# Performance work log

Hardware: AMD Instinct MI355X
Metric: run time of the kernel (lower is better)

## Reference

```python
import jax, jax.numpy as jnp
import numpy as np

B, N, C, H = 2, 4096, 256, 4
DH = C // H  # 64
EPS = 1e-6
TEMPERATURE = 1.0


def setup_inputs() -> dict:
    key = jax.random.key(0)
    ks = jax.random.split(key, 12)
    s = 0.02
    return {
        "x": jax.random.normal(ks[0], (B, N, C), dtype=jnp.float32),
        "pos_embed": jax.random.normal(ks[1], (B, N, C), dtype=jnp.float32),
        # per-head Q/K/V linear weights stacked over heads (torch Linear(dim, dim_head))
        "Wq": jax.random.normal(ks[2], (H, C, DH), dtype=jnp.float32) * s,
        "bq": jax.random.normal(ks[3], (H, DH), dtype=jnp.float32) * s,
        "Wk": jax.random.normal(ks[4], (H, C, DH), dtype=jnp.float32) * s,
        "bk": jax.random.normal(ks[5], (H, DH), dtype=jnp.float32) * s,
        "Wv": jax.random.normal(ks[6], (H, C, DH), dtype=jnp.float32) * s,
        "bv": jax.random.normal(ks[7], (H, DH), dtype=jnp.float32) * s,
        "Wo": jax.random.normal(ks[8], (C, C), dtype=jnp.float32) * s,
        "bo": jax.random.normal(ks[9], (C,), dtype=jnp.float32) * s,
        "ln_g": jnp.ones((C,), dtype=jnp.float32),
        "ln_b": jnp.zeros((C,), dtype=jnp.float32),
    }


def reference(x, pos_embed, Wq, bq, Wk, bk, Wv, bv, Wo, bo, ln_g, ln_b):
    dk = TEMPERATURE * jnp.sqrt(jnp.float32(DH))
    # pre-norm: x + pos_embed -> dropout(p=0, identity) -> LayerNorm(eps=1e-6)
    h = x + pos_embed
    mu = jnp.mean(h, axis=-1, keepdims=True)
    var = jnp.mean(jnp.square(h - mu), axis=-1, keepdims=True)
    h = (h - mu) * jax.lax.rsqrt(var + EPS) * ln_g + ln_b  # [B,N,C]
    # all heads at once (original loops over heads with separate small Linears)
    q = jnp.einsum("bnc,hcd->bhnd", h, Wq) + bq[None, :, None, :]
    k = jnp.einsum("bnc,hcd->bhnd", h, Wk) + bk[None, :, None, :]
    v = jnp.einsum("bnc,hcd->bhnd", h, Wv) + bv[None, :, None, :]
    scores = jnp.einsum("bhid,bhjd->bhij", q, k) / dk  # [B,H,N,N]
    # NOTE: original uses F.softmax(dot_prod, dim=1) on [B,N,N] -> normalize over
    # the QUERY axis i, not the key axis j. Replicated faithfully here (axis=2).
    attn = jax.nn.softmax(scores, axis=2)
    o = jnp.einsum("bhij,bhjd->bhid", attn, v)  # [B,H,N,DH]
    o = jnp.transpose(o, (0, 2, 1, 3)).reshape(B, N, C)  # concat heads on channel
    return o @ Wo + bo
```

## Files before the change

kernel.cpp:

```cpp
#include <hip/hip_runtime.h>
#include <math.h>

#define B_ 2
#define N_ 4096
#define C_ 256
#define H_ 4
#define DH_ 64
#define EPS_ 1e-6f
#define SCALE_Q_ 0.18033688011112042f

typedef short bf16x8 __attribute__((ext_vector_type(8)));
typedef short bf16x4v __attribute__((ext_vector_type(4)));
typedef float f32x4 __attribute__((ext_vector_type(4)));
typedef int i32x4 __attribute__((ext_vector_type(4)));

#define MFMA32(a, b, c) __builtin_amdgcn_mfma_f32_16x16x32_bf16(a, b, c, 0, 0, 0)
#define FAST_EXP2(x) __builtin_amdgcn_exp2f(x)

__device__ __forceinline__ unsigned short f2bf(float x) {
  unsigned int u = __float_as_uint(x);
  return (unsigned short)((u + 0x7FFFu + ((u >> 16) & 1u)) >> 16);
}
__device__ __forceinline__ float bf2f(unsigned short u) {
  return __uint_as_float(((unsigned int)u) << 16);
}
__device__ __forceinline__ int pack2bf(float lo, float hi) {
  return (int)__builtin_amdgcn_perm(__float_as_uint(hi) + 0x8000u,
                                    __float_as_uint(lo) + 0x8000u, 0x07060302u);
}

__global__ __launch_bounds__(256) void ln_kernel(
    const float* __restrict__ x, const float* __restrict__ pos,
    const float* __restrict__ g, const float* __restrict__ beta,
    unsigned short* __restrict__ h16) {
  const int w = threadIdx.x >> 6, lane = threadIdx.x & 63;
  const int row = blockIdx.x * 4 + w;
  const float4 xv = *(const float4*)&x[row * C_ + lane * 4];
  const float4 pv = *(const float4*)&pos[row * C_ + lane * 4];
  float4 v = {xv.x + pv.x, xv.y + pv.y, xv.z + pv.z, xv.w + pv.w};
  float s = v.x + v.y + v.z + v.w;
  s += __shfl_xor(s, 1);  s += __shfl_xor(s, 2);  s += __shfl_xor(s, 4);
  s += __shfl_xor(s, 8);  s += __shfl_xor(s, 16); s += __shfl_xor(s, 32);
  const float mu = s * (1.0f / C_);
  float4 d = {v.x - mu, v.y - mu, v.z - mu, v.w - mu};
  float q = d.x * d.x + d.y * d.y + d.z * d.z + d.w * d.w;
  q += __shfl_xor(q, 1);  q += __shfl_xor(q, 2);  q += __shfl_xor(q, 4);
  q += __shfl_xor(q, 8);  q += __shfl_xor(q, 16); q += __shfl_xor(q, 32);
  const float rs = rsqrtf(q * (1.0f / C_) + EPS_);
  const float4 g4 = *(const float4*)&g[lane * 4];
  const float4 b4 = *(const float4*)&beta[lane * 4];
  bf16x4v o;
  o[0] = (short)f2bf(d.x * rs * g4.x + b4.x);
  o[1] = (short)f2bf(d.y * rs * g4.y + b4.y);
  o[2] = (short)f2bf(d.z * rs * g4.z + b4.z);
  o[3] = (short)f2bf(d.w * rs * g4.w + b4.w);
  *(bf16x4v*)&h16[row * C_ + lane * 4] = o;
}

__global__ __launch_bounds__(256) void wconv_kernel(
    const float* __restrict__ Wq, const float* __restrict__ Wk,
    const float* __restrict__ Wv, const float* __restrict__ Wo,
    unsigned short* __restrict__ W3T, unsigned short* __restrict__ WoT) {
  const int base = blockIdx.x * 2048;
#pragma unroll
  for (int p = 0; p < 8; p++) {
    const int idx = base + p * 256 + threadIdx.x;
    if (idx < 196608) {
      const int m = idx >> 14;
      const int rem = idx & 16383;
      const int c = rem >> 6, d = rem & 63;
      const int h = m / 3, kind = m - h * 3;
      const float* W = kind == 0 ? Wq : kind == 1 ? Wk : Wv;
      float v = W[h * 16384 + rem];
      if (kind == 0) v *= SCALE_Q_;
      W3T[(h * 192 + kind * 64 + d) * 256 + c] = f2bf(v);
    } else {
      const int widx = idx - 196608;
      const int k = widx >> 8, n = widx & 255;
      WoT[n * 256 + k] = f2bf(Wo[widx]);
    }
  }
}

__global__ __launch_bounds__(256) void qkv_kernel(
    const unsigned short* __restrict__ h16, const unsigned short* __restrict__ W3T,
    const float* __restrict__ bq, const float* __restrict__ bk,
    const float* __restrict__ bv,
    unsigned short* __restrict__ q16, unsigned short* __restrict__ k16,
    unsigned short* __restrict__ vT16) {
  const int rt = blockIdx.x;
  const int hh = blockIdx.y;
  const int t = threadIdx.x;
  const int w = t >> 6, lane = t & 63, c = lane & 15, quad = lane >> 4;
  __shared__ unsigned short Hs[64 * 64];
  __shared__ unsigned short Bs[192 * 64];
  const int row0 = rt * 64;

  f32x4 acc[12];
#pragma unroll
  for (int nt = 0; nt < 12; nt++) acc[nt] = (f32x4){0.f, 0.f, 0.f, 0.f};

  for (int kt = 0; kt < C_; kt += 64) {
    __syncthreads();
#pragma unroll
    for (int p = 0; p < 2; p++) {
      const int e = t + p * 256;
      const int row = e >> 3, ch = e & 7;
      *(bf16x8*)&Hs[row * 64 + ((ch ^ (row & 7)) * 8)] =
          *(const bf16x8*)&h16[(size_t)(row0 + row) * C_ + kt + ch * 8];
    }
#pragma unroll
    for (int p = 0; p < 6; p++) {
      const int e = t + p * 256;
      const int row = e >> 3, ch = e & 7;
      *(bf16x8*)&Bs[row * 64 + ((ch ^ (row & 7)) * 8)] =
          *(const bf16x8*)&W3T[(size_t)(hh * 192 + row) * C_ + kt + ch * 8];
    }
    __syncthreads();
#pragma unroll
    for (int kh = 0; kh < 2; kh++) {
      const int i = w * 16 + c;
      bf16x8 a = *(const bf16x8*)&Hs[i * 64 + (((kh * 4 + quad) ^ (i & 7)) * 8)];
#pragma unroll
      for (int nt = 0; nt < 12; nt++) {
        const int n = nt * 16 + c;
        bf16x8 b = *(const bf16x8*)&Bs[n * 64 + (((kh * 4 + quad) ^ (n & 7)) * 8)];
        acc[nt] = MFMA32(a, b, acc[nt]);
      }
    }
  }
#pragma unroll
  for (int nt = 0; nt < 12; nt++) {
    const int kind = nt >> 2;
    const int col = (nt & 3) * 16 + c;
    const float bias = kind == 0 ? bq[hh * 64 + col] * SCALE_Q_
                     : kind == 1 ? bk[hh * 64 + col] : bv[hh * 64 + col];
#pragma unroll
    for (int r = 0; r < 4; r++) {
      const int gr = row0 + w * 16 + quad * 4 + r;
      const int b = gr >> 12, n = gr & (N_ - 1);
      const size_t bh = (size_t)(b * H_ + hh);
      const unsigned short val = f2bf(acc[nt][r] + bias);
      if (kind == 0)      q16[(bh * N_ + n) * DH_ + col] = val;
      else if (kind == 1) k16[(bh * N_ + n) * DH_ + col] = val;
      else                vT16[(bh * DH_ + col) * N_ + n] = val;
    }
  }
}

__global__ __launch_bounds__(256, 2) void colstats_kernel(
    const unsigned short* __restrict__ q16, const unsigned short* __restrict__ k16,
    unsigned short* __restrict__ vT16) {
  const int blk = blockIdx.x;
  const int bh = blk & 7;
  const int j0 = (blk >> 3) * 64;
  const int t = threadIdx.x;
  const int w = t >> 6, lane = t & 63, c = lane & 15, quad = lane >> 4;
  __shared__ unsigned short Qs[64 * 64];
  __shared__ float Lp[4][64];
  __shared__ float ilv[64];

  bf16x8 ka[4][2];
#pragma unroll
  for (int jb = 0; jb < 4; jb++) {
    const size_t kb = ((size_t)bh * N_ + j0 + jb * 16 + c) * DH_;
    ka[jb][0] = *(const bf16x8*)&k16[kb + quad * 8];
    ka[jb][1] = *(const bf16x8*)&k16[kb + 32 + quad * 8];
  }

  bf16x8 pre[2];
  auto loadQ = [&](int i0) {
#pragma unroll
    for (int p = 0; p < 2; p++) {
      const int e = t + p * 256;
      const int row = e >> 3, ch = e & 7;
      pre[p] = *(const bf16x8*)&q16[((size_t)bh * N_ + i0 + row) * DH_ + ch * 8];
    }
  };
  loadQ(0);

  f32x4 lsum[4];
#pragma unroll
  for (int jb = 0; jb < 4; jb++) lsum[jb] = (f32x4){0.f, 0.f, 0.f, 0.f};

  for (int i0 = 0; i0 < N_; i0 += 64) {
    __syncthreads();
#pragma unroll
    for (int p = 0; p < 2; p++) {
      const int e = t + p * 256;
      const int row = e >> 3, ch = e & 7;
      *(bf16x8*)&Qs[row * 64 + ((ch ^ (row & 7)) * 8)] = pre[p];
    }
    __syncthreads();
    if (i0 + 64 < N_) loadQ(i0 + 64);
    const int ir = w * 16 + c;
    bf16x8 qf0 = *(const bf16x8*)&Qs[ir * 64 + ((quad ^ (c & 7)) * 8)];
    bf16x8 qf1 = *(const bf16x8*)&Qs[ir * 64 + (((4 + quad) ^ (c & 7)) * 8)];
#pragma unroll
    for (int jb = 0; jb < 4; jb++) {
      f32x4 s = {0.f, 0.f, 0.f, 0.f};
      s = MFMA32(ka[jb][0], qf0, s);
      s = MFMA32(ka[jb][1], qf1, s);
#pragma unroll
      for (int r = 0; r < 4; r++) lsum[jb][r] += FAST_EXP2(s[r]);
    }
  }
#pragma unroll
  for (int jb = 0; jb < 4; jb++) {
#pragma unroll
    for (int r = 0; r < 4; r++) {
      float s = lsum[jb][r];
      s += __shfl_xor(s, 1); s += __shfl_xor(s, 2);
      s += __shfl_xor(s, 4); s += __shfl_xor(s, 8);
      if (c == 0) Lp[w][jb * 16 + quad * 4 + r] = s;
    }
  }
  __syncthreads();
  if (t < 64) ilv[t] = 1.0f / (Lp[0][t] + Lp[1][t] + Lp[2][t] + Lp[3][t]);
  __syncthreads();
#pragma unroll
  for (int p = 0; p < 2; p++) {
    const int e = t + p * 256;
    const int d = e >> 3, ch = e & 7;
    const size_t addr = ((size_t)bh * DH_ + d) * N_ + j0 + ch * 8;
    bf16x8 v = *(const bf16x8*)&vT16[addr];
#pragma unroll
    for (int jj = 0; jj < 8; jj++)
      v[jj] = (short)f2bf(bf2f((unsigned short)v[jj]) * ilv[ch * 8 + jj]);
    *(bf16x8*)&vT16[addr] = v;
  }
}

__global__ __launch_bounds__(512, 4) void attnout_kernel(
    const unsigned short* __restrict__ q16, const unsigned short* __restrict__ k16,
    const unsigned short* __restrict__ vT16, unsigned short* __restrict__ ob16) {
  const int blk = blockIdx.x;
  const int bh = blk & 7;
  const int bb = bh >> 2, hh = bh & 3;
  const int i0 = (blk >> 3) * 64;
  const int t = threadIdx.x;
  const int w = t >> 6, lane = t & 63, c = lane & 15, quad = lane >> 4;
  const int iw = w >> 2;
  const int jw = w & 3;

  __shared__ __align__(16) char smem[32768];
  unsigned short* Ks = (unsigned short*)smem;
  unsigned short* Vs = (unsigned short*)smem + 128 * 64;
  float* Rf = (float*)smem;

  bf16x8 qa[2][2];
#pragma unroll
  for (int ib = 0; ib < 2; ib++) {
    const size_t qb = ((size_t)bh * N_ + i0 + iw * 32 + ib * 16 + c) * DH_;
    qa[ib][0] = *(const bf16x8*)&q16[qb + quad * 8];
    qa[ib][1] = *(const bf16x8*)&q16[qb + 32 + quad * 8];
  }

  bf16x8 kpre[2], vpre[2];
  auto loadKV = [&](int jt) {
#pragma unroll
    for (int p = 0; p < 2; p++) {
      const int e = t + p * 512;
      kpre[p] = *(const bf16x8*)&k16[((size_t)bh * N_ + jt + (e >> 3)) * DH_ + (e & 7) * 8];
      vpre[p] = *(const bf16x8*)&vT16[((size_t)bh * DH_ + (e >> 4)) * N_ + jt + (e & 15) * 8];
    }
  };
  loadKV(0);

  f32x4 of[2][4];
#pragma unroll
  for (int ib = 0; ib < 2; ib++)
#pragma unroll
    for (int dt = 0; dt < 4; dt++) of[ib][dt] = (f32x4){0.f, 0.f, 0.f, 0.f};

  for (int jt = 0; jt < N_; jt += 128) {
    __syncthreads();
#pragma unroll
    for (int p = 0; p < 2; p++) {
      const int e = t + p * 512;
      { const int row = e >> 3, ch = e & 7;
        *(bf16x8*)&Ks[row * 64 + ((ch ^ ((row >> 2) & 7)) * 8)] = kpre[p]; }
      { const int d = e >> 4, ch = e & 15;
        *(bf16x8*)&Vs[d * 128 + ((ch ^ (d & 15)) * 8)] = vpre[p]; }
    }
    __syncthreads();
    if (jt + 128 < N_) loadKV(jt + 128);

    bf16x8 kf[2][2];
#pragma unroll
    for (int s = 0; s < 2; s++) {
      const int jr = jw * 32 + ((c >> 2) * 8) + s * 4 + (c & 3);
      const int swz = (jr >> 2) & 7;
      kf[s][0] = *(const bf16x8*)&Ks[jr * 64 + ((quad ^ swz) * 8)];
      kf[s][1] = *(const bf16x8*)&Ks[jr * 64 + (((4 + quad) ^ swz) * 8)];
    }
    bf16x8 vf[4];
#pragma unroll
    for (int dt = 0; dt < 4; dt++) {
      const int d = dt * 16 + c;
      vf[dt] = *(const bf16x8*)&Vs[d * 128 + (((jw * 4 + quad) ^ (d & 15)) * 8)];
    }

#pragma unroll
    for (int ib = 0; ib < 2; ib++) {
      f32x4 s0 = {0.f, 0.f, 0.f, 0.f}, s1 = {0.f, 0.f, 0.f, 0.f};
      s0 = MFMA32(kf[0][0], qa[ib][0], s0);
      s0 = MFMA32(kf[0][1], qa[ib][1], s0);
      s1 = MFMA32(kf[1][0], qa[ib][0], s1);
      s1 = MFMA32(kf[1][1], qa[ib][1], s1);
      i32x4 pi;
      pi[0] = pack2bf(FAST_EXP2(s0[0]), FAST_EXP2(s0[1]));
      pi[1] = pack2bf(FAST_EXP2(s0[2]), FAST_EXP2(s0[3]));
      pi[2] = pack2bf(FAST_EXP2(s1[0]), FAST_EXP2(s1[1]));
      pi[3] = pack2bf(FAST_EXP2(s1[2]), FAST_EXP2(s1[3]));
      bf16x8 pf = *(bf16x8*)&pi;
#pragma unroll
      for (int dt = 0; dt < 4; dt++)
        of[ib][dt] = MFMA32(pf, vf[dt], of[ib][dt]);
    }
  }

  __syncthreads();
  if (jw >= 2) {
    float* dst = Rf + (iw * 2 + (jw - 2)) * 2048;
#pragma unroll
    for (int ib = 0; ib < 2; ib++)
#pragma unroll
      for (int dt = 0; dt < 4; dt++)
        *(f32x4*)&dst[lane * 32 + (((ib * 4 + dt) ^ (lane & 7)) * 4)] = of[ib][dt];
  }
  __syncthreads();
  if (jw < 2) {
    const float* src = Rf + (iw * 2 + jw) * 2048;
#pragma unroll
    for (int ib = 0; ib < 2; ib++)
#pragma unroll
      for (int dt = 0; dt < 4; dt++)
        of[ib][dt] += *(const f32x4*)&src[lane * 32 + (((ib * 4 + dt) ^ (lane & 7)) * 4)];
  }
  __syncthreads();
  if (jw == 1) {
    float* dst = Rf + iw * 2048;
#pragma unroll
    for (int ib = 0; ib < 2; ib++)
#pragma unroll
      for (int dt = 0; dt < 4; dt++)
        *(f32x4*)&dst[lane * 32 + (((ib * 4 + dt) ^ (lane & 7)) * 4)] = of[ib][dt];
  }
  __syncthreads();
  if (jw == 0) {
    const float* src = Rf + iw * 2048;
#pragma unroll
    for (int ib = 0; ib < 2; ib++)
#pragma unroll
      for (int dt = 0; dt < 4; dt++) {
        of[ib][dt] += *(const f32x4*)&src[lane * 32 + (((ib * 4 + dt) ^ (lane & 7)) * 4)];
#pragma unroll
        for (int r = 0; r < 4; r++)
          ob16[((size_t)bb * N_ + i0 + iw * 32 + ib * 16 + quad * 4 + r) * C_ +
               hh * DH_ + dt * 16 + c] = f2bf(of[ib][dt][r]);
      }
  }
}

__global__ __launch_bounds__(256) void outproj_kernel(
    const unsigned short* __restrict__ ob16, const unsigned short* __restrict__ WoT,
    const float* __restrict__ bo, float* __restrict__ out) {
  const int rt = blockIdx.x;
  const int t = threadIdx.x;
  const int w = t >> 6, lane = t & 63, c = lane & 15, quad = lane >> 4;
  __shared__ unsigned short As[32 * 64];
  __shared__ unsigned short Bs[256 * 64];

  f32x4 acc[2][4];
#pragma unroll
  for (int mt = 0; mt < 2; mt++)
#pragma unroll
    for (int nt = 0; nt < 4; nt++) acc[mt][nt] = (f32x4){0.f, 0.f, 0.f, 0.f};

  for (int kt = 0; kt < C_; kt += 64) {
    __syncthreads();
    {
      const int row = t >> 3, ch = t & 7;
      *(bf16x8*)&As[row * 64 + ((ch ^ (row & 7)) * 8)] =
          *(const bf16x8*)&ob16[((size_t)rt * 32 + row) * C_ + kt + ch * 8];
    }
#pragma unroll
    for (int p = 0; p < 8; p++) {
      const int e = t + p * 256;
      const int row = e >> 3, ch = e & 7;
      *(bf16x8*)&Bs[row * 64 + ((ch ^ (row & 7)) * 8)] =
          *(const bf16x8*)&WoT[(size_t)row * C_ + kt + ch * 8];
    }
    __syncthreads();
#pragma unroll
    for (int kh = 0; kh < 2; kh++) {
      bf16x8 a[2];
#pragma unroll
      for (int mt = 0; mt < 2; mt++) {
        const int i = mt * 16 + c;
        a[mt] = *(const bf16x8*)&As[i * 64 + (((kh * 4 + quad) ^ (i & 7)) * 8)];
      }
#pragma unroll
      for (int nt = 0; nt < 4; nt++) {
        const int n = w * 64 + nt * 16 + c;
        bf16x8 b = *(const bf16x8*)&Bs[n * 64 + (((kh * 4 + quad) ^ (n & 7)) * 8)];
        acc[0][nt] = MFMA32(a[0], b, acc[0][nt]);
        acc[1][nt] = MFMA32(a[1], b, acc[1][nt]);
      }
    }
  }
#pragma unroll
  for (int mt = 0; mt < 2; mt++)
#pragma unroll
    for (int nt = 0; nt < 4; nt++) {
      const int col = w * 64 + nt * 16 + c;
      const float bias = bo[col];
#pragma unroll
      for (int r = 0; r < 4; r++)
        out[((size_t)rt * 32 + mt * 16 + quad * 4 + r) * C_ + col] = acc[mt][nt][r] + bias;
    }
}

extern "C" void kernel_launch(void* const* d_in, const int* in_sizes, int n_in,
                              void* d_out, int out_size, void* d_ws, size_t ws_size,
                              hipStream_t stream) {
  const float* x    = (const float*)d_in[0];
  const float* pos  = (const float*)d_in[1];
  const float* Wq   = (const float*)d_in[2];
  const float* bq   = (const float*)d_in[3];
  const float* Wk   = (const float*)d_in[4];
  const float* bk   = (const float*)d_in[5];
  const float* Wv   = (const float*)d_in[6];
  const float* bv   = (const float*)d_in[7];
  const float* Wo   = (const float*)d_in[8];
  const float* bo   = (const float*)d_in[9];
  const float* ln_g = (const float*)d_in[10];
  const float* ln_b = (const float*)d_in[11];
  float* out = (float*)d_out;

  const size_t SZ = (size_t)B_ * N_ * C_;
  unsigned short* h16  = (unsigned short*)d_ws;
  unsigned short* q16  = h16 + SZ;
  unsigned short* k16  = q16 + SZ;
  unsigned short* vT16 = k16 + SZ;
  unsigned short* ob16 = vT16 + SZ;
  unsigned short* W3T  = ob16 + SZ;
  unsigned short* WoT  = W3T + (size_t)H_ * 192 * 256;

  ln_kernel<<<B_ * N_ / 4, 256, 0, stream>>>(x, pos, ln_g, ln_b, h16);
  wconv_kernel<<<128, 256, 0, stream>>>(Wq, Wk, Wv, Wo, W3T, WoT);
  qkv_kernel<<<dim3(128, H_), 256, 0, stream>>>(h16, W3T, bq, bk, bv, q16, k16, vT16);
  colstats_kernel<<<512, 256, 0, stream>>>(q16, k16, vT16);
  attnout_kernel<<<512, 512, 0, stream>>>(q16, k16, vT16, ob16);
  outproj_kernel<<<256, 256, 0, stream>>>(ob16, WoT, bo, out);
}
```

Measured before the change: 187.3 us.

## Fuse LayerNorm into QKV projection and split out-projection columns across blocks

The separate LayerNorm kernel is removed. Each QKV block now computes LayerNorm for its 64 rows straight from x and pos, using a single-pass sum/sum-of-squares variance, and keeps the full normalized bf16 tile in shared memory. This drops one launch and the h16 round trip through global memory, but each of the 4 head blocks recomputes the same rows' LayerNorm, and Hs grows to 32KB. The output projection is also split over two column halves, which doubles the grid to 512 blocks so more CUs are busy.

```diff
diff --git a/kernel.cpp b/kernel.cpp
--- a/kernel.cpp
+++ b/kernel.cpp
@@ -10,7 +10,6 @@
 #define SCALE_Q_ 0.18033688011112042f
 
 typedef short bf16x8 __attribute__((ext_vector_type(8)));
-typedef short bf16x4v __attribute__((ext_vector_type(4)));
 typedef float f32x4 __attribute__((ext_vector_type(4)));
 typedef int i32x4 __attribute__((ext_vector_type(4)));
 
@@ -27,34 +26,6 @@
 __device__ __forceinline__ int pack2bf(float lo, float hi) {
   return (int)__builtin_amdgcn_perm(__float_as_uint(hi) + 0x8000u,
                                     __float_as_uint(lo) + 0x8000u, 0x07060302u);
-}
-
-__global__ __launch_bounds__(256) void ln_kernel(
-    const float* __restrict__ x, const float* __restrict__ pos,
-    const float* __restrict__ g, const float* __restrict__ beta,
-    unsigned short* __restrict__ h16) {
-  const int w = threadIdx.x >> 6, lane = threadIdx.x & 63;
-  const int row = blockIdx.x * 4 + w;
-  const float4 xv = *(const float4*)&x[row * C_ + lane * 4];
-  const float4 pv = *(const float4*)&pos[row * C_ + lane * 4];
-  float4 v = {xv.x + pv.x, xv.y + pv.y, xv.z + pv.z, xv.w + pv.w};
-  float s = v.x + v.y + v.z + v.w;
-  s += __shfl_xor(s, 1);  s += __shfl_xor(s, 2);  s += __shfl_xor(s, 4);
-  s += __shfl_xor(s, 8);  s += __shfl_xor(s, 16); s += __shfl_xor(s, 32);
-  const float mu = s * (1.0f / C_);
-  float4 d = {v.x - mu, v.y - mu, v.z - mu, v.w - mu};
-  float q = d.x * d.x + d.y * d.y + d.z * d.z + d.w * d.w;
-  q += __shfl_xor(q, 1);  q += __shfl_xor(q, 2);  q += __shfl_xor(q, 4);
-  q += __shfl_xor(q, 8);  q += __shfl_xor(q, 16); q += __shfl_xor(q, 32);
-  const float rs = rsqrtf(q * (1.0f / C_) + EPS_);
-  const float4 g4 = *(const float4*)&g[lane * 4];
-  const float4 b4 = *(const float4*)&beta[lane * 4];
-  bf16x4v o;
-  o[0] = (short)f2bf(d.x * rs * g4.x + b4.x);
-  o[1] = (short)f2bf(d.y * rs * g4.y + b4.y);
-  o[2] = (short)f2bf(d.z * rs * g4.z + b4.z);
-  o[3] = (short)f2bf(d.w * rs * g4.w + b4.w);
-  *(bf16x4v*)&h16[row * C_ + lane * 4] = o;
 }
 
 __global__ __launch_bounds__(256) void wconv_kernel(
@@ -82,8 +53,10 @@
   }
 }
 
-__global__ __launch_bounds__(256) void qkv_kernel(
-    const unsigned short* __restrict__ h16, const unsigned short* __restrict__ W3T,
+__global__ __launch_bounds__(256) void qkvln_kernel(
+    const float* __restrict__ x, const float* __restrict__ pos,
+    const float* __restrict__ g, const float* __restrict__ beta,
+    const unsigned short* __restrict__ W3T,
     const float* __restrict__ bq, const float* __restrict__ bk,
     const float* __restrict__ bv,
     unsigned short* __restrict__ q16, unsigned short* __restrict__ k16,
@@ -92,35 +65,70 @@
   const int hh = blockIdx.y;
   const int t = threadIdx.x;
   const int w = t >> 6, lane = t & 63, c = lane & 15, quad = lane >> 4;
-  __shared__ unsigned short Hs[64 * 64];
+  __shared__ unsigned short Hs[4 * 64 * 64];
   __shared__ unsigned short Bs[192 * 64];
   const int row0 = rt * 64;
 
+  {
+    const int lrow = t >> 2, seg = t & 3;
+    const size_t base = (size_t)(row0 + lrow) * C_ + seg * 64;
+    float sum = 0.f, ssq = 0.f;
+#pragma unroll
+    for (int k4 = 0; k4 < 16; k4++) {
+      const float4 xv = *(const float4*)&x[base + k4 * 4];
+      const float4 pv = *(const float4*)&pos[base + k4 * 4];
+      const float v0 = xv.x + pv.x, v1 = xv.y + pv.y;
+      const float v2 = xv.z + pv.z, v3 = xv.w + pv.w;
+      sum += v0 + v1 + v2 + v3;
+      ssq += v0 * v0 + v1 * v1 + v2 * v2 + v3 * v3;
+    }
+    sum += __shfl_xor(sum, 1); sum += __shfl_xor(sum, 2);
+    ssq += __shfl_xor(ssq, 1); ssq += __shfl_xor(ssq, 2);
+    const float mu = sum * (1.0f / C_);
+    const float var = fmaxf(ssq * (1.0f / C_) - mu * mu, 0.0f);
+    const float rs = rsqrtf(var + EPS_);
+#pragma unroll
+    for (int k8 = 0; k8 < 8; k8++) {
+      const float4 xa = *(const float4*)&x[base + k8 * 8];
+      const float4 pa = *(const float4*)&pos[base + k8 * 8];
+      const float4 xb = *(const float4*)&x[base + k8 * 8 + 4];
+      const float4 pb = *(const float4*)&pos[base + k8 * 8 + 4];
+      const float4 ga = *(const float4*)&g[seg * 64 + k8 * 8];
+      const float4 gb = *(const float4*)&g[seg * 64 + k8 * 8 + 4];
+      const float4 ba = *(const float4*)&beta[seg * 64 + k8 * 8];
+      const float4 bb = *(const float4*)&beta[seg * 64 + k8 * 8 + 4];
+      bf16x8 o;
+      o[0] = (short)f2bf((xa.x + pa.x - mu) * rs * ga.x + ba.x);
+      o[1] = (short)f2bf((xa.y + pa.y - mu) * rs * ga.y + ba.y);
+      o[2] = (short)f2bf((xa.z + pa.z - mu) * rs * ga.z + ba.z);
+      o[3] = (short)f2bf((xa.w + pa.w - mu) * rs * ga.w + ba.w);
+      o[4] = (short)f2bf((xb.x + pb.x - mu) * rs * gb.x + bb.x);
+      o[5] = (short)f2bf((xb.y + pb.y - mu) * rs * gb.y + bb.y);
+      o[6] = (short)f2bf((xb.z + pb.z - mu) * rs * gb.z + bb.z);
+      o[7] = (short)f2bf((xb.w + pb.w - mu) * rs * gb.w + bb.w);
+      *(bf16x8*)&Hs[seg * 4096 + lrow * 64 + ((k8 ^ (lrow & 7)) * 8)] = o;
+    }
+  }
+  __syncthreads();
+
   f32x4 acc[12];
 #pragma unroll
   for (int nt = 0; nt < 12; nt++) acc[nt] = (f32x4){0.f, 0.f, 0.f, 0.f};
 
-  for (int kt = 0; kt < C_; kt += 64) {
-    __syncthreads();
-#pragma unroll
-    for (int p = 0; p < 2; p++) {
-      const int e = t + p * 256;
-      const int row = e >> 3, ch = e & 7;
-      *(bf16x8*)&Hs[row * 64 + ((ch ^ (row & 7)) * 8)] =
-          *(const bf16x8*)&h16[(size_t)(row0 + row) * C_ + kt + ch * 8];
-    }
+  for (int kt4 = 0; kt4 < 4; kt4++) {
+    __syncthreads();
 #pragma unroll
     for (int p = 0; p < 6; p++) {
       const int e = t + p * 256;
       const int row = e >> 3, ch = e & 7;
       *(bf16x8*)&Bs[row * 64 + ((ch ^ (row & 7)) * 8)] =
-          *(const bf16x8*)&W3T[(size_t)(hh * 192 + row) * C_ + kt + ch * 8];
+          *(const bf16x8*)&W3T[(size_t)(hh * 192 + row) * C_ + kt4 * 64 + ch * 8];
     }
     __syncthreads();
 #pragma unroll
     for (int kh = 0; kh < 2; kh++) {
       const int i = w * 16 + c;
-      bf16x8 a = *(const bf16x8*)&Hs[i * 64 + (((kh * 4 + quad) ^ (i & 7)) * 8)];
+      bf16x8 a = *(const bf16x8*)&Hs[kt4 * 4096 + i * 64 + (((kh * 4 + quad) ^ (i & 7)) * 8)];
 #pragma unroll
       for (int nt = 0; nt < 12; nt++) {
         const int n = nt * 16 + c;
@@ -367,16 +375,17 @@
     const unsigned short* __restrict__ ob16, const unsigned short* __restrict__ WoT,
     const float* __restrict__ bo, float* __restrict__ out) {
   const int rt = blockIdx.x;
+  const int ch2 = blockIdx.y;
   const int t = threadIdx.x;
   const int w = t >> 6, lane = t & 63, c = lane & 15, quad = lane >> 4;
   __shared__ unsigned short As[32 * 64];
-  __shared__ unsigned short Bs[256 * 64];
-
-  f32x4 acc[2][4];
+  __shared__ unsigned short Bs[128 * 64];
+
+  f32x4 acc[2][2];
 #pragma unroll
   for (int mt = 0; mt < 2; mt++)
 #pragma unroll
-    for (int nt = 0; nt < 4; nt++) acc[mt][nt] = (f32x4){0.f, 0.f, 0.f, 0.f};
+    for (int nt = 0; nt < 2; nt++) acc[mt][nt] = (f32x4){0.f, 0.f, 0.f, 0.f};
 
   for (int kt = 0; kt < C_; kt += 64) {
     __syncthreads();
@@ -386,11 +395,11 @@
           *(const bf16x8*)&ob16[((size_t)rt * 32 + row) * C_ + kt + ch * 8];
     }
 #pragma unroll
-    for (int p = 0; p < 8; p++) {
+    for (int p = 0; p < 4; p++) {
       const int e = t + p * 256;
       const int row = e >> 3, ch = e & 7;
       *(bf16x8*)&Bs[row * 64 + ((ch ^ (row & 7)) * 8)] =
-          *(const bf16x8*)&WoT[(size_t)row * C_ + kt + ch * 8];
+          *(const bf16x8*)&WoT[(size_t)(ch2 * 128 + row) * C_ + kt + ch * 8];
     }
     __syncthreads();
 #pragma unroll
@@ -402,8 +411,8 @@
         a[mt] = *(const bf16x8*)&As[i * 64 + (((kh * 4 + quad) ^ (i & 7)) * 8)];
       }
 #pragma unroll
-      for (int nt = 0; nt < 4; nt++) {
-        const int n = w * 64 + nt * 16 + c;
+      for (int nt = 0; nt < 2; nt++) {
+        const int n = w * 32 + nt * 16 + c;
         bf16x8 b = *(const bf16x8*)&Bs[n * 64 + (((kh * 4 + quad) ^ (n & 7)) * 8)];
         acc[0][nt] = MFMA32(a[0], b, acc[0][nt]);
         acc[1][nt] = MFMA32(a[1], b, acc[1][nt]);
@@ -413,8 +422,8 @@
 #pragma unroll
   for (int mt = 0; mt < 2; mt++)
 #pragma unroll
-    for (int nt = 0; nt < 4; nt++) {
-      const int col = w * 64 + nt * 16 + c;
+    for (int nt = 0; nt < 2; nt++) {
+      const int col = ch2 * 128 + w * 32 + nt * 16 + c;
       const float bias = bo[col];
 #pragma unroll
       for (int r = 0; r < 4; r++)
@@ -440,18 +449,17 @@
   float* out = (float*)d_out;
 
   const size_t SZ = (size_t)B_ * N_ * C_;
-  unsigned short* h16  = (unsigned short*)d_ws;
-  unsigned short* q16  = h16 + SZ;
+  unsigned short* q16  = (unsigned short*)d_ws;
   unsigned short* k16  = q16 + SZ;
   unsigned short* vT16 = k16 + SZ;
   unsigned short* ob16 = vT16 + SZ;
   unsigned short* W3T  = ob16 + SZ;
   unsigned short* WoT  = W3T + (size_t)H_ * 192 * 256;
 
-  ln_kernel<<<B_ * N_ / 4, 256, 0, stream>>>(x, pos, ln_g, ln_b, h16);
   wconv_kernel<<<128, 256, 0, stream>>>(Wq, Wk, Wv, Wo, W3T, WoT);
-  qkv_kernel<<<dim3(128, H_), 256, 0, stream>>>(h16, W3T, bq, bk, bv, q16, k16, vT16);
+  qkvln_kernel<<<dim3(128, H_), 256, 0, stream>>>(
+      x, pos, ln_g, ln_b, W3T, bq, bk, bv, q16, k16, vT16);
   colstats_kernel<<<512, 256, 0, stream>>>(q16, k16, vT16);
   attnout_kernel<<<512, 512, 0, stream>>>(q16, k16, vT16, ob16);
-  outproj_kernel<<<256, 256, 0, stream>>>(ob16, WoT, bo, out);
-}
+  outproj_kernel<<<dim3(256, 2), 256, 0, stream>>>(ob16, WoT, bo, out);
+}
```

New measurement: 232.2 us. +24.0%, slower.
